# Performance work log

Hardware: AMD Instinct MI355X
Metric: run time of the kernel (lower is better)

The kernel has to match this reference:

```python
import jax, jax.numpy as jnp
import numpy as np

N_WIN = 8
NUM_HEADS = 8
TOPK = 4
D_MODEL = 128
SCALE = D_MODEL ** (-0.5)


def setup_inputs() -> dict:
    key = jax.random.key(0)
    k1, k2 = jax.random.split(key)
    cv_feature = jax.random.normal(k1, (1, 128, 128, 128), dtype=jnp.float32)
    mv_feature = jax.random.normal(k2, (1, 2, 128, 128, 128), dtype=jnp.float32)
    return {"cv_feature": cv_feature, "mv_feature": mv_feature}


def reference(cv_feature, mv_feature):
    # cv_feature: [N, H, W, C] query view; mv_feature: [N, V, H, W, C] multi-view KV
    N, H, W, C = cv_feature.shape
    V = mv_feature.shape[1]
    j = i = N_WIN
    h, w = H // j, W // i
    p2, w2 = j * i, h * w
    ch = C // NUM_HEADS  # per-head dim

    # window partition: n (j h) (i w) c -> n (j i) h w c
    cv_patch = cv_feature.reshape(N, j, h, i, w, C).transpose(0, 1, 3, 2, 4, 5).reshape(N, p2, h, w, C)
    mv_patch = mv_feature.reshape(N, V, j, h, i, w, C).transpose(0, 1, 2, 4, 3, 5, 6).reshape(N, V, p2, h, w, C)

    q_pix = cv_patch.reshape(N, p2, w2, C)          # [N, p2, w2, C]
    kv_pix = mv_patch.reshape(N, V, p2, w2, C)      # [N, V, p2, w2, C]

    # window-level descriptors (means) -> routing logits
    q_win = cv_patch.mean(axis=(2, 3))              # [N, p2, C]
    k_win = mv_patch.mean(axis=(3, 4))              # [N, V, p2, C]

    # TopK routing (detached in original; forward math identical)
    k_flat = k_win.reshape(N, V * p2, C)
    attn_logit = jnp.einsum('npc,nqc->npq', q_win * SCALE, k_flat)  # [N, p2, V*p2]
    topk_logit, r_idx = jax.lax.top_k(attn_logit, TOPK)
    r_weight = jax.nn.softmax(topk_logit, axis=-1)  # computed by module, unused downstream

    # KV gather of selected windows: [N, p2, topk, w2, C]
    kv_flat = kv_pix.reshape(N, V * p2, w2, C)
    kv_sel = kv_flat[jnp.arange(N)[:, None, None], r_idx]

    # per-window multi-head attention over topk*w2 gathered tokens
    q = q_pix.reshape(N, p2, w2, NUM_HEADS, ch)
    kv = kv_sel.reshape(N, p2, TOPK * w2, NUM_HEADS, ch)
    attn = jnp.einsum('npwmc,npxmc->npmwx', q * SCALE, kv)  # [N, p2, m, w2, topk*w2]
    attn = jax.nn.softmax(attn, axis=-1)
    out = jnp.einsum('npmwx,npxmc->npwmc', attn, kv)        # [N, p2, w2, m, ch]

    # merge windows back: n (j i) (h w) c -> n (j h) (i w) c
    out = out.reshape(N, j, i, h, w, C).transpose(0, 1, 3, 2, 4, 5).reshape(N, H, W, C)
    return out
```

## Files before the change

### kernel.cpp

```cpp
#include <hip/hip_runtime.h>

#define HH_ 128
#define WW_ 128
#define CC_ 128
#define P2 64
#define W2 256
#define NH 8
#define CH 16
#define NV 2
#define TOPK 4
#define SCALE 0.08838834764831845f
#define SCALE_L2E 0.1275216f
#define CLAMP_L2 28.8539f

typedef unsigned short u16;
typedef unsigned int   u32;
typedef short s8v __attribute__((ext_vector_type(8)));
typedef float f4  __attribute__((ext_vector_type(4)));

#if __has_builtin(__builtin_amdgcn_exp2f)
#define EXP2(x) __builtin_amdgcn_exp2f(x)
#else
#define EXP2(x) exp2f(x)
#endif

union FRAG { uint4 q; u32 u[4]; s8v v; };

__device__ float g_means[(P2 + NV * P2) * CC_];
__device__ int2  g_part[64];

__device__ inline u16 f2b(float v) {
    union { float f; u32 u; } x; x.f = v;
    u32 r = x.u + 0x7FFFu + ((x.u >> 16) & 1u);
    return (u16)(r >> 16);
}
__device__ inline float b2f(u16 h) {
    union { u32 u; float f; } x; x.u = (u32)h << 16; return x.f;
}
__device__ inline float h2f(u16 h) {
    u32 s = (h >> 15) & 1u, e = (h >> 10) & 31u, m = h & 1023u;
    float v;
    if (e == 0)       v = m * 5.9604644775e-8f;
    else if (e == 31) v = 65504.f;
    else { union { u32 u; float f; } x; x.u = ((e + 112u) << 23) | (m << 13); v = x.f; }
    return s ? -v : v;
}
__device__ inline u16 f2h(float v) {
    union { float f; u32 u; } x; x.f = v;
    u32 s = (x.u >> 16) & 0x8000u;
    int  e = (int)((x.u >> 23) & 0xFF) - 112;
    u32  m = x.u & 0x7FFFFF;
    if (e >= 31) return (u16)(s | 0x7BFF);
    if (e <= 0) {
        if (e < -10) return (u16)s;
        m |= 0x800000u;
        int sh = 14 - e;
        u32 r = m >> sh, rem = m & ((1u << sh) - 1u), half = 1u << (sh - 1);
        if (rem > half || (rem == half && (r & 1))) r++;
        return (u16)(s | r);
    }
    u32 r = ((u32)e << 10) | (m >> 13), rem = m & 0x1FFFu;
    if (rem > 0x1000u || (rem == 0x1000u && (r & 1))) r++;
    return (u16)(s | r);
}

__device__ inline u32 pkhi(float a, float b) {
    union { float f; u32 u; } xa, xb; xa.f = a; xb.f = b;
    return (xa.u >> 16) | (xb.u & 0xFFFF0000u);
}
__device__ inline float hipart(float a) {
    union { float f; u32 u; } x; x.f = a; x.u &= 0xFFFF0000u; return x.f;
}

__device__ inline int mode_from_parts() {
    int c0 = 0, c1 = 0;
#pragma unroll 8
    for (int k = 0; k < 64; ++k) { int2 v = g_part[k]; c0 += v.x; c1 += v.y; }
    const float T = 256.f * 64.f;
    float f0 = c0 / T, f1 = c1 / T;
    if (f1 >= 0.85f) return 1;
    if (f0 >= 0.80f) return 0;
    return 2;
}

template<int MODE>
__device__ inline float decode1(const void* __restrict__ src, int off) {
    if (MODE == 0) return ((const float*)src)[off];
    u16 h = ((const u16*)src)[off];
    return (MODE == 1) ? b2f(h) : h2f(h);
}

template<int MODE>
__device__ inline float4 loadf4(const void* __restrict__ src, int off) {
    if (MODE == 0) return *(const float4*)((const float*)src + off);
    uint2 v = *(const uint2*)((const u16*)src + off);
    float4 r;
    if (MODE == 1) {
        r.x = b2f((u16)v.x); r.y = b2f((u16)(v.x >> 16));
        r.z = b2f((u16)v.y); r.w = b2f((u16)(v.y >> 16));
    } else {
        r.x = h2f((u16)v.x); r.y = h2f((u16)(v.x >> 16));
        r.z = h2f((u16)v.y); r.w = h2f((u16)(v.y >> 16));
    }
    return r;
}

template<int MODE>
__device__ inline void store4t(void* __restrict__ out, int off, const float* __restrict__ r) {
    if (MODE == 0) {
        *(float4*)((float*)out + off) = make_float4(r[0], r[1], r[2], r[3]);
    } else if (MODE == 1) {
        u32 w0 = (u32)f2b(r[0]) | ((u32)f2b(r[1]) << 16);
        u32 w1 = (u32)f2b(r[2]) | ((u32)f2b(r[3]) << 16);
        *(uint2*)((u16*)out + off) = make_uint2(w0, w1);
    } else {
        u32 w0 = (u32)f2h(r[0]) | ((u32)f2h(r[1]) << 16);
        u32 w1 = (u32)f2h(r[2]) | ((u32)f2h(r[3]) << 16);
        *(uint2*)((u16*)out + off) = make_uint2(w0, w1);
    }
}

__global__ void detect_sample(const void* __restrict__ cv, int n) {
    __shared__ int bc[2];
    int tid = threadIdx.x, k = blockIdx.x;
    if (tid < 2) bc[tid] = 0;
    __syncthreads();
    int lim32 = n / 2;
    int lim16 = n / 2;
    u32 r = ((u32)(tid + k * 257) * 2654435761u);
    int j32 = (int)(r % (u32)lim32);
    float a = fabsf(((const float*)cv)[j32]);
    bool c0 = (a >= 1e-4f && a <= 1e4f);
    int j16 = 2 * (int)((r >> 8) % (u32)lim16);
    float b = fabsf(b2f(((const u16*)cv)[j16]));
    bool c1 = (b >= 1e-4f && b <= 1e4f);
    unsigned long long b0 = __ballot(c0);
    unsigned long long b1 = __ballot(c1);
    if ((tid & 63) == 0) {
        atomicAdd(&bc[0], __popcll(b0));
        atomicAdd(&bc[1], __popcll(b1));
    }
    __syncthreads();
    if (tid == 0) g_part[k] = make_int2(bc[0], bc[1]);
}

template<int MODE>
__device__ inline void wm_accum(const void* __restrict__ src, int voff, int jj, int ii,
                                int pc, int c0, float* __restrict__ acc) {
#pragma unroll
    for (int k = 0; k < 8; ++k) {
        int px = 8 * pc + k;
        int hh = px >> 4, ww = px & 15;
        int a = voff + ((jj * 16 + hh) * WW_ + ii * 16 + ww) * CC_ + c0;
        if (MODE == 0) {
            const float4* p4 = (const float4*)((const float*)src + a);
            float4 x = p4[0], y = p4[1];
            acc[0] += x.x; acc[1] += x.y; acc[2] += x.z; acc[3] += x.w;
            acc[4] += y.x; acc[5] += y.y; acc[6] += y.z; acc[7] += y.w;
        } else {
            uint4 v = *(const uint4*)((const u16*)src + a);
            u32 wd[4] = { v.x, v.y, v.z, v.w };
#pragma unroll
            for (int j = 0; j < 4; ++j) {
                u16 lo = (u16)(wd[j] & 0xFFFFu), hi = (u16)(wd[j] >> 16);
                acc[2 * j]     += (MODE == 1) ? b2f(lo) : h2f(lo);
                acc[2 * j + 1] += (MODE == 1) ? b2f(hi) : h2f(hi);
            }
        }
    }
}

__global__ __launch_bounds__(512) void win_mean_kernel(const void* __restrict__ cv,
                                                       const void* __restrict__ mv) {
    __shared__ float part[32][128];
    __shared__ int   smode;
    int row = blockIdx.x, tid = threadIdx.x;
    if (tid == 0) smode = mode_from_parts();
    __syncthreads();
    int mode = smode;
    int o = tid & 15, pc = tid >> 4;
    const void* src; int voff = 0; int p;
    if (row < P2) { p = row; src = cv; }
    else { int r = row - P2; voff = (r >> 6) * HH_ * WW_ * CC_; p = r & 63; src = mv; }
    int jj = p >> 3, ii = p & 7;
    int c0 = 8 * o;
    float acc[8];
#pragma unroll
    for (int j = 0; j < 8; ++j) acc[j] = 0.f;
    if (mode == 0)      wm_accum<0>(src, voff, jj, ii, pc, c0, acc);
    else if (mode == 1) wm_accum<1>(src, voff, jj, ii, pc, c0, acc);
    else                wm_accum<2>(src, voff, jj, ii, pc, c0, acc);
#pragma unroll
    for (int j = 0; j < 8; ++j) part[pc][c0 + j] = acc[j];
    __syncthreads();
    if (tid < 128) {
        float s = 0.f;
#pragma unroll
        for (int k = 0; k < 32; ++k) s += part[k][tid];
        g_means[row * CC_ + tid] = s * (1.0f / 256.0f);
    }
}

template<int MODE>
__device__ void attn_body(const void* __restrict__ cv, const void* __restrict__ mv,
                          void* __restrict__ out, int p, int m, int tid,
                          u32 (* __restrict__ kfrag)[64][4],
                          u32 (* __restrict__ vfrag)[64][4],
                          const int* __restrict__ rwin) {
    int jj = p >> 3, ii = p & 7;
    int wv = tid >> 6, l = tid & 63;
    int kh = wv >> 3, qs = wv & 7;
    int lg = l >> 4, lr = l & 15;

    FRAG qf1[2], qf2[2];
#pragma unroll
    for (int qi = 0; qi < 2; ++qi) {
        int qrow = qs * 32 + qi * 16 + lr;
        int hh = qrow >> 4, ww = qrow & 15;
        int pix = (jj * 16 + hh) * WW_ + (ii * 16 + ww);
        float4 qv = loadf4<MODE>(cv, pix * CC_ + m * CH + 4 * lg);
        float q0 = qv.x * SCALE_L2E, q1 = qv.y * SCALE_L2E;
        float q2 = qv.z * SCALE_L2E, q3 = qv.w * SCALE_L2E;
        u32 h01 = pkhi(q0, q1), h23 = pkhi(q2, q3);
        u32 l01 = pkhi(q0 - hipart(q0), q1 - hipart(q1));
        u32 l23 = pkhi(q2 - hipart(q2), q3 - hipart(q3));
        qf1[qi].u[0] = h01; qf1[qi].u[1] = h23; qf1[qi].u[2] = l01; qf1[qi].u[3] = l23;
        qf2[qi].u[0] = l01; qf2[qi].u[1] = l23; qf2[qi].u[2] = h01; qf2[qi].u[3] = h23;
    }

    auto stage = [&](int r) {
#pragma unroll
        for (int i = 0; i < 2; ++i) {
            int s = tid + i * 1024;
            int tl = s >> 6, sl = s & 63;
            int slg = sl >> 4, slr = sl & 15;
            int t = rwin[2 * r + (tl >> 4)];
            int v = t >> 6, pp = t & 63;
            int jj2 = pp >> 3, ii2 = pp & 7;
            int wrow = (v * HH_ + jj2 * 16 + (tl & 15)) * WW_ + ii2 * 16;
            {
                float4 kc = loadf4<MODE>(mv, (wrow + slr) * CC_ + m * CH + 4 * slg);
                FRAG kf;
                kf.u[0] = pkhi(kc.x, kc.y);
                kf.u[1] = pkhi(kc.z, kc.w);
                kf.u[2] = pkhi(kc.x - hipart(kc.x), kc.y - hipart(kc.y));
                kf.u[3] = pkhi(kc.z - hipart(kc.z), kc.w - hipart(kc.w));
                *(uint4*)&kfrag[tl][sl][0] = kf.q;
            }
            {
                int a = (wrow + 4 * slg) * CC_ + m * CH + slr;
                float v0 = decode1<MODE>(mv, a);
                float v1 = decode1<MODE>(mv, a + CC_);
                float v2 = decode1<MODE>(mv, a + 2 * CC_);
                float v3 = decode1<MODE>(mv, a + 3 * CC_);
                FRAG vf;
                vf.u[0] = pkhi(v0, v1);
                vf.u[1] = pkhi(v2, v3);
                vf.u[2] = pkhi(v0 - hipart(v0), v1 - hipart(v1));
                vf.u[3] = pkhi(v2 - hipart(v2), v3 - hipart(v3));
                *(uint4*)&vfrag[tl][sl][0] = vf.q;
            }
        }
    };

    f4 Oacc0 = {0.f, 0.f, 0.f, 0.f};
    f4 Oacc1 = {0.f, 0.f, 0.f, 0.f};
    float lp0 = 0.f, lp1 = 0.f;
    const uint4* kp = (const uint4*)&kfrag[kh * 16][0][0] + l;
    const uint4* vp = (const uint4*)&vfrag[kh * 16][0][0] + l;

    auto computeh = [&]() {
#pragma unroll 4
        for (int tl = 0; tl < 16; ++tl) {
            FRAG kf, vf;
            kf.q = kp[tl * 64];
            vf.q = vp[tl * 64];
            {
                f4 sc = {0.f, 0.f, 0.f, 0.f};
                sc = __builtin_amdgcn_mfma_f32_16x16x32_bf16(kf.v, qf1[0].v, sc, 0, 0, 0);
                sc = __builtin_amdgcn_mfma_f32_16x16x32_bf16(kf.v, qf2[0].v, sc, 0, 0, 0);
                float pe0 = EXP2(fminf(sc[0], CLAMP_L2));
                float pe1 = EXP2(fminf(sc[1], CLAMP_L2));
                float pe2 = EXP2(fminf(sc[2], CLAMP_L2));
                float pe3 = EXP2(fminf(sc[3], CLAMP_L2));
                lp0 += (hipart(pe0) + hipart(pe1)) + (hipart(pe2) + hipart(pe3));
                FRAG pf;
                pf.u[0] = pkhi(pe0, pe1);
                pf.u[1] = pkhi(pe2, pe3);
                pf.u[2] = pf.u[0];
                pf.u[3] = pf.u[1];
                Oacc0 = __builtin_amdgcn_mfma_f32_16x16x32_bf16(vf.v, pf.v, Oacc0, 0, 0, 0);
            }
            {
                f4 sc = {0.f, 0.f, 0.f, 0.f};
                sc = __builtin_amdgcn_mfma_f32_16x16x32_bf16(kf.v, qf1[1].v, sc, 0, 0, 0);
                sc = __builtin_amdgcn_mfma_f32_16x16x32_bf16(kf.v, qf2[1].v, sc, 0, 0, 0);
                float pe0 = EXP2(fminf(sc[0], CLAMP_L2));
                float pe1 = EXP2(fminf(sc[1], CLAMP_L2));
                float pe2 = EXP2(fminf(sc[2], CLAMP_L2));
                float pe3 = EXP2(fminf(sc[3], CLAMP_L2));
                lp1 += (hipart(pe0) + hipart(pe1)) + (hipart(pe2) + hipart(pe3));
                FRAG pf;
                pf.u[0] = pkhi(pe0, pe1);
                pf.u[1] = pkhi(pe2, pe3);
                pf.u[2] = pf.u[0];
                pf.u[3] = pf.u[1];
                Oacc1 = __builtin_amdgcn_mfma_f32_16x16x32_bf16(vf.v, pf.v, Oacc1, 0, 0, 0);
            }
        }
    };

    stage(0);
    __syncthreads();
    computeh();
    __syncthreads();
    stage(1);
    __syncthreads();
    computeh();
    __syncthreads();

    float* comb = (float*)&kfrag[0][0][0];
    int ci = (qs * 64 + l) * 10;
    if (kh == 1) {
#pragma unroll
        for (int r = 0; r < 4; ++r) { comb[ci + r] = Oacc0[r]; comb[ci + 4 + r] = Oacc1[r]; }
        comb[ci + 8] = lp0;
        comb[ci + 9] = lp1;
    }
    __syncthreads();
    if (kh == 0) {
#pragma unroll
        for (int r = 0; r < 4; ++r) { Oacc0[r] += comb[ci + r]; Oacc1[r] += comb[ci + 4 + r]; }
        lp0 += comb[ci + 8];
        lp1 += comb[ci + 9];
#pragma unroll
        for (int qi = 0; qi < 2; ++qi) {
            float lt = (qi == 0) ? lp0 : lp1;
            lt += __shfl_xor(lt, 16);
            lt += __shfl_xor(lt, 32);
            float inv = 1.0f / fmaxf(lt, 1e-30f);
            f4 Oa = (qi == 0) ? Oacc0 : Oacc1;
            float res[4];
#pragma unroll
            for (int r = 0; r < 4; ++r)
                res[r] = fminf(fmaxf(Oa[r] * inv, -1000.f), 1000.f);
            int qrow = qs * 32 + qi * 16 + lr;
            int hh = qrow >> 4, ww = qrow & 15;
            int pix = (jj * 16 + hh) * WW_ + (ii * 16 + ww);
            store4t<MODE>(out, pix * CC_ + m * CH + 4 * lg, res);
        }
    }
}

__global__ __launch_bounds__(1024, 8) void attn_kernel(const void* __restrict__ cv,
                                                       const void* __restrict__ mv,
                                                       void* __restrict__ out) {
    __shared__ u32 kfrag[32][64][4];
    __shared__ u32 vfrag[32][64][4];
    __shared__ float slog[NV * P2];
    __shared__ int   sridx[TOPK];
    __shared__ int   smode;

    int bid = blockIdx.x;
    int p = bid >> 3, m = bid & 7;
    int tid = threadIdx.x;

    {
        int t  = tid >> 3;
        int cs = (tid & 7) << 4;
        const float4* qw = (const float4*)(g_means + p * CC_ + cs);
        const float4* kw = (const float4*)(g_means + (P2 + t) * CC_ + cs);
        float a = 0.f;
#pragma unroll
        for (int i = 0; i < 4; ++i) {
            float4 qv = qw[i], kv4 = kw[i];
            a += qv.x * kv4.x + qv.y * kv4.y + qv.z * kv4.z + qv.w * kv4.w;
        }
        a += __shfl_down(a, 4, 8);
        a += __shfl_down(a, 2, 8);
        a += __shfl_down(a, 1, 8);
        if ((tid & 7) == 0) slog[t] = a;
    }
    __syncthreads();
    if (tid == 0) {
        smode = mode_from_parts();
#pragma unroll
        for (int k = 0; k < TOPK; ++k) {
            int best = 0; float bv = slog[0];
            for (int q2 = 1; q2 < NV * P2; ++q2)
                if (slog[q2] > bv) { bv = slog[q2]; best = q2; }
            sridx[k] = best;
            slog[best] = -3.0e38f;
        }
    }
    __syncthreads();

    int mode = smode;
    int rwin[TOPK];
#pragma unroll
    for (int k = 0; k < TOPK; ++k) rwin[k] = sridx[k] & 127;

    if (mode == 0)      attn_body<0>(cv, mv, out, p, m, tid, kfrag, vfrag, rwin);
    else if (mode == 1) attn_body<1>(cv, mv, out, p, m, tid, kfrag, vfrag, rwin);
    else                attn_body<2>(cv, mv, out, p, m, tid, kfrag, vfrag, rwin);
}

extern "C" void kernel_launch(void* const* d_in, const int* in_sizes, int n_in,
                              void* d_out, int out_size, void* d_ws, size_t ws_size,
                              hipStream_t stream) {
    const void* cv = d_in[0];
    const void* mv = d_in[1];
    int n_cv = in_sizes[0];
    if (n_in >= 2 && in_sizes[0] > in_sizes[1]) { cv = d_in[1]; mv = d_in[0]; n_cv = in_sizes[1]; }
    (void)d_ws; (void)ws_size; (void)out_size;

    detect_sample<<<64, 256, 0, stream>>>(cv, n_cv);
    win_mean_kernel<<<192, 512, 0, stream>>>(cv, mv);
    attn_kernel<<<P2 * NH, 1024, 0, stream>>>(cv, mv, d_out);
}
```

Measured before the change: 129.9 us.

## Fuse dtype detection, window means, and attention into one kernel with grid barriers

Merges the three launches (dtype sampling, window-mean reduction, routed attention) into a single persistent kernel. Global atomic counters in workspace act as grid-wide barriers between the phases, and a memset resets them on each call. This removes inter-kernel launch gaps at the cost of spin-waiting on atomics. It assumes all 512 blocks of 1024 threads are co-resident, otherwise the barriers can deadlock.

```diff
diff --git a/kernel.cpp b/kernel.cpp
--- a/kernel.cpp
+++ b/kernel.cpp
@@ -117,87 +117,6 @@
         u32 w0 = (u32)f2h(r[0]) | ((u32)f2h(r[1]) << 16);
         u32 w1 = (u32)f2h(r[2]) | ((u32)f2h(r[3]) << 16);
         *(uint2*)((u16*)out + off) = make_uint2(w0, w1);
-    }
-}
-
-__global__ void detect_sample(const void* __restrict__ cv, int n) {
-    __shared__ int bc[2];
-    int tid = threadIdx.x, k = blockIdx.x;
-    if (tid < 2) bc[tid] = 0;
-    __syncthreads();
-    int lim32 = n / 2;
-    int lim16 = n / 2;
-    u32 r = ((u32)(tid + k * 257) * 2654435761u);
-    int j32 = (int)(r % (u32)lim32);
-    float a = fabsf(((const float*)cv)[j32]);
-    bool c0 = (a >= 1e-4f && a <= 1e4f);
-    int j16 = 2 * (int)((r >> 8) % (u32)lim16);
-    float b = fabsf(b2f(((const u16*)cv)[j16]));
-    bool c1 = (b >= 1e-4f && b <= 1e4f);
-    unsigned long long b0 = __ballot(c0);
-    unsigned long long b1 = __ballot(c1);
-    if ((tid & 63) == 0) {
-        atomicAdd(&bc[0], __popcll(b0));
-        atomicAdd(&bc[1], __popcll(b1));
-    }
-    __syncthreads();
-    if (tid == 0) g_part[k] = make_int2(bc[0], bc[1]);
-}
-
-template<int MODE>
-__device__ inline void wm_accum(const void* __restrict__ src, int voff, int jj, int ii,
-                                int pc, int c0, float* __restrict__ acc) {
-#pragma unroll
-    for (int k = 0; k < 8; ++k) {
-        int px = 8 * pc + k;
-        int hh = px >> 4, ww = px & 15;
-        int a = voff + ((jj * 16 + hh) * WW_ + ii * 16 + ww) * CC_ + c0;
-        if (MODE == 0) {
-            const float4* p4 = (const float4*)((const float*)src + a);
-            float4 x = p4[0], y = p4[1];
-            acc[0] += x.x; acc[1] += x.y; acc[2] += x.z; acc[3] += x.w;
-            acc[4] += y.x; acc[5] += y.y; acc[6] += y.z; acc[7] += y.w;
-        } else {
-            uint4 v = *(const uint4*)((const u16*)src + a);
-            u32 wd[4] = { v.x, v.y, v.z, v.w };
-#pragma unroll
-            for (int j = 0; j < 4; ++j) {
-                u16 lo = (u16)(wd[j] & 0xFFFFu), hi = (u16)(wd[j] >> 16);
-                acc[2 * j]     += (MODE == 1) ? b2f(lo) : h2f(lo);
-                acc[2 * j + 1] += (MODE == 1) ? b2f(hi) : h2f(hi);
-            }
-        }
-    }
-}
-
-__global__ __launch_bounds__(512) void win_mean_kernel(const void* __restrict__ cv,
-                                                       const void* __restrict__ mv) {
-    __shared__ float part[32][128];
-    __shared__ int   smode;
-    int row = blockIdx.x, tid = threadIdx.x;
-    if (tid == 0) smode = mode_from_parts();
-    __syncthreads();
-    int mode = smode;
-    int o = tid & 15, pc = tid >> 4;
-    const void* src; int voff = 0; int p;
-    if (row < P2) { p = row; src = cv; }
-    else { int r = row - P2; voff = (r >> 6) * HH_ * WW_ * CC_; p = r & 63; src = mv; }
-    int jj = p >> 3, ii = p & 7;
-    int c0 = 8 * o;
-    float acc[8];
-#pragma unroll
-    for (int j = 0; j < 8; ++j) acc[j] = 0.f;
-    if (mode == 0)      wm_accum<0>(src, voff, jj, ii, pc, c0, acc);
-    else if (mode == 1) wm_accum<1>(src, voff, jj, ii, pc, c0, acc);
-    else                wm_accum<2>(src, voff, jj, ii, pc, c0, acc);
-#pragma unroll
-    for (int j = 0; j < 8; ++j) part[pc][c0 + j] = acc[j];
-    __syncthreads();
-    if (tid < 128) {
-        float s = 0.f;
-#pragma unroll
-        for (int k = 0; k < 32; ++k) s += part[k][tid];
-        g_means[row * CC_ + tid] = s * (1.0f / 256.0f);
     }
 }
 
@@ -352,6 +271,235 @@
     }
 }
 
+template<int MODE>
+__device__ inline void wm_row(const void* __restrict__ cv, const void* __restrict__ mv,
+                              int row, int tid, float (* __restrict__ wmpart)[128]) {
+    int o = tid & 15, pc = tid >> 4;
+    const void* src; int voff = 0; int p;
+    if (row < P2) { p = row; src = cv; }
+    else { int r = row - P2; voff = (r >> 6) * HH_ * WW_ * CC_; p = r & 63; src = mv; }
+    int jj = p >> 3, ii = p & 7;
+    int c0 = 8 * o;
+    float acc[8];
+#pragma unroll
+    for (int j = 0; j < 8; ++j) acc[j] = 0.f;
+#pragma unroll
+    for (int k = 0; k < 4; ++k) {
+        int px = 4 * pc + k;
+        int hh = px >> 4, ww = px & 15;
+        int a = voff + ((jj * 16 + hh) * WW_ + ii * 16 + ww) * CC_ + c0;
+        if (MODE == 0) {
+            const float4* p4 = (const float4*)((const float*)src + a);
+            float4 x = p4[0], y = p4[1];
+            acc[0] += x.x; acc[1] += x.y; acc[2] += x.z; acc[3] += x.w;
+            acc[4] += y.x; acc[5] += y.y; acc[6] += y.z; acc[7] += y.w;
+        } else {
+            uint4 v = *(const uint4*)((const u16*)src + a);
+            u32 wd[4] = { v.x, v.y, v.z, v.w };
+#pragma unroll
+            for (int j = 0; j < 4; ++j) {
+                u16 lo = (u16)(wd[j] & 0xFFFFu), hi = (u16)(wd[j] >> 16);
+                acc[2 * j]     += (MODE == 1) ? b2f(lo) : h2f(lo);
+                acc[2 * j + 1] += (MODE == 1) ? b2f(hi) : h2f(hi);
+            }
+        }
+    }
+#pragma unroll
+    for (int j = 0; j < 8; ++j) wmpart[pc][c0 + j] = acc[j];
+}
+
+__global__ __launch_bounds__(1024, 8) void fused_kernel(const void* __restrict__ cv,
+                                                        const void* __restrict__ mv,
+                                                        void* __restrict__ out,
+                                                        int* __restrict__ cnt, int n) {
+    __shared__ u32 kfrag[32][64][4];
+    __shared__ u32 vfrag[32][64][4];
+    __shared__ float slog[NV * P2];
+    __shared__ int   sridx[TOPK];
+    __shared__ int   smode;
+    __shared__ int   bc[2];
+
+    int bid = blockIdx.x, tid = threadIdx.x;
+    int p = bid >> 3, m = bid & 7;
+
+    if (bid < 64) {
+        if (tid < 2) bc[tid] = 0;
+        __syncthreads();
+        if (tid < 256) {
+            int lim = n / 2;
+            u32 r = ((u32)(tid + bid * 257) * 2654435761u);
+            int j32 = (int)(r % (u32)lim);
+            float a = fabsf(((const float*)cv)[j32]);
+            bool c0 = (a >= 1e-4f && a <= 1e4f);
+            int j16 = 2 * (int)((r >> 8) % (u32)lim);
+            float b = fabsf(b2f(((const u16*)cv)[j16]));
+            bool c1 = (b >= 1e-4f && b <= 1e4f);
+            unsigned long long b0 = __ballot(c0);
+            unsigned long long b1 = __ballot(c1);
+            if ((tid & 63) == 0) {
+                atomicAdd(&bc[0], __popcll(b0));
+                atomicAdd(&bc[1], __popcll(b1));
+            }
+        }
+        __syncthreads();
+        if (tid == 0) {
+            atomicAdd(&cnt[2], bc[0]);
+            atomicAdd(&cnt[3], bc[1]);
+            __threadfence();
+            atomicAdd(&cnt[0], 1);
+        }
+    }
+    if (tid == 0) {
+        while (atomicAdd(&cnt[0], 0) < 64) { __builtin_amdgcn_s_sleep(2); }
+        int c0s = atomicAdd(&cnt[2], 0);
+        int c1s = atomicAdd(&cnt[3], 0);
+        const float T = 256.f * 64.f;
+        float f0 = c0s / T, f1 = c1s / T;
+        smode = (f1 >= 0.85f) ? 1 : ((f0 >= 0.80f) ? 0 : 2);
+    }
+    __syncthreads();
+    int mode = smode;
+
+    if (bid < 192) {
+        float (*wmpart)[128] = (float(*)[128])&kfrag[0][0][0];
+        if (mode == 0)      wm_row<0>(cv, mv, bid, tid, wmpart);
+        else if (mode == 1) wm_row<1>(cv, mv, bid, tid, wmpart);
+        else                wm_row<2>(cv, mv, bid, tid, wmpart);
+        __syncthreads();
+        if (tid < 128) {
+            float s = 0.f;
+#pragma unroll
+            for (int k = 0; k < 64; ++k) s += wmpart[k][tid];
+            g_means[bid * CC_ + tid] = s * (1.0f / 256.0f);
+        }
+        __threadfence();
+        __syncthreads();
+        if (tid == 0) atomicAdd(&cnt[1], 1);
+    }
+    if (tid == 0) {
+        while (atomicAdd(&cnt[1], 0) < 192) { __builtin_amdgcn_s_sleep(2); }
+        __threadfence();
+    }
+    __syncthreads();
+
+    {
+        int t  = tid >> 3;
+        int cs = (tid & 7) << 4;
+        const float4* qw = (const float4*)(g_means + p * CC_ + cs);
+        const float4* kw = (const float4*)(g_means + (P2 + t) * CC_ + cs);
+        float a = 0.f;
+#pragma unroll
+        for (int i = 0; i < 4; ++i) {
+            float4 qv = qw[i], kv4 = kw[i];
+            a += qv.x * kv4.x + qv.y * kv4.y + qv.z * kv4.z + qv.w * kv4.w;
+        }
+        a += __shfl_down(a, 4, 8);
+        a += __shfl_down(a, 2, 8);
+        a += __shfl_down(a, 1, 8);
+        if ((tid & 7) == 0) slog[t] = a;
+    }
+    __syncthreads();
+    if (tid == 0) {
+#pragma unroll
+        for (int k = 0; k < TOPK; ++k) {
+            int best = 0; float bv = slog[0];
+            for (int q2 = 1; q2 < NV * P2; ++q2)
+                if (slog[q2] > bv) { bv = slog[q2]; best = q2; }
+            sridx[k] = best;
+            slog[best] = -3.0e38f;
+        }
+    }
+    __syncthreads();
+
+    int rwin[TOPK];
+#pragma unroll
+    for (int k = 0; k < TOPK; ++k) rwin[k] = sridx[k] & 127;
+
+    if (mode == 0)      attn_body<0>(cv, mv, out, p, m, tid, kfrag, vfrag, rwin);
+    else if (mode == 1) attn_body<1>(cv, mv, out, p, m, tid, kfrag, vfrag, rwin);
+    else                attn_body<2>(cv, mv, out, p, m, tid, kfrag, vfrag, rwin);
+}
+
+__global__ void detect_sample(const void* __restrict__ cv, int n) {
+    __shared__ int bc[2];
+    int tid = threadIdx.x, k = blockIdx.x;
+    if (tid < 2) bc[tid] = 0;
+    __syncthreads();
+    int lim = n / 2;
+    u32 r = ((u32)(tid + k * 257) * 2654435761u);
+    int j32 = (int)(r % (u32)lim);
+    float a = fabsf(((const float*)cv)[j32]);
+    bool c0 = (a >= 1e-4f && a <= 1e4f);
+    int j16 = 2 * (int)((r >> 8) % (u32)lim);
+    float b = fabsf(b2f(((const u16*)cv)[j16]));
+    bool c1 = (b >= 1e-4f && b <= 1e4f);
+    unsigned long long b0 = __ballot(c0);
+    unsigned long long b1 = __ballot(c1);
+    if ((tid & 63) == 0) {
+        atomicAdd(&bc[0], __popcll(b0));
+        atomicAdd(&bc[1], __popcll(b1));
+    }
+    __syncthreads();
+    if (tid == 0) g_part[k] = make_int2(bc[0], bc[1]);
+}
+
+template<int MODE>
+__device__ inline void wm_accum(const void* __restrict__ src, int voff, int jj, int ii,
+                                int pc, int c0, float* __restrict__ acc) {
+#pragma unroll
+    for (int k = 0; k < 8; ++k) {
+        int px = 8 * pc + k;
+        int hh = px >> 4, ww = px & 15;
+        int a = voff + ((jj * 16 + hh) * WW_ + ii * 16 + ww) * CC_ + c0;
+        if (MODE == 0) {
+            const float4* p4 = (const float4*)((const float*)src + a);
+            float4 x = p4[0], y = p4[1];
+            acc[0] += x.x; acc[1] += x.y; acc[2] += x.z; acc[3] += x.w;
+            acc[4] += y.x; acc[5] += y.y; acc[6] += y.z; acc[7] += y.w;
+        } else {
+            uint4 v = *(const uint4*)((const u16*)src + a);
+            u32 wd[4] = { v.x, v.y, v.z, v.w };
+#pragma unroll
+            for (int j = 0; j < 4; ++j) {
+                u16 lo = (u16)(wd[j] & 0xFFFFu), hi = (u16)(wd[j] >> 16);
+                acc[2 * j]     += (MODE == 1) ? b2f(lo) : h2f(lo);
+                acc[2 * j + 1] += (MODE == 1) ? b2f(hi) : h2f(hi);
+            }
+        }
+    }
+}
+
+__global__ __launch_bounds__(512) void win_mean_kernel2(const void* __restrict__ cv,
+                                                        const void* __restrict__ mv) {
+    __shared__ float part[32][128];
+    __shared__ int   smode;
+    int row = blockIdx.x, tid = threadIdx.x;
+    if (tid == 0) smode = mode_from_parts();
+    __syncthreads();
+    int mode = smode;
+    int o = tid & 15, pc = tid >> 4;
+    const void* src; int voff = 0; int p;
+    if (row < P2) { p = row; src = cv; }
+    else { int r = row - P2; voff = (r >> 6) * HH_ * WW_ * CC_; p = r & 63; src = mv; }
+    int jj = p >> 3, ii = p & 7;
+    int c0 = 8 * o;
+    float acc[8];
+#pragma unroll
+    for (int j = 0; j < 8; ++j) acc[j] = 0.f;
+    if (mode == 0)      wm_accum<0>(src, voff, jj, ii, pc, c0, acc);
+    else if (mode == 1) wm_accum<1>(src, voff, jj, ii, pc, c0, acc);
+    else                wm_accum<2>(src, voff, jj, ii, pc, c0, acc);
+#pragma unroll
+    for (int j = 0; j < 8; ++j) part[pc][c0 + j] = acc[j];
+    __syncthreads();
+    if (tid < 128) {
+        float s = 0.f;
+#pragma unroll
+        for (int k = 0; k < 32; ++k) s += part[k][tid];
+        g_means[row * CC_ + tid] = s * (1.0f / 256.0f);
+    }
+}
+
 __global__ __launch_bounds__(1024, 8) void attn_kernel(const void* __restrict__ cv,
                                                        const void* __restrict__ mv,
                                                        void* __restrict__ out) {
@@ -412,9 +560,15 @@
     const void* mv = d_in[1];
     int n_cv = in_sizes[0];
     if (n_in >= 2 && in_sizes[0] > in_sizes[1]) { cv = d_in[1]; mv = d_in[0]; n_cv = in_sizes[1]; }
-    (void)d_ws; (void)ws_size; (void)out_size;
-
-    detect_sample<<<64, 256, 0, stream>>>(cv, n_cv);
-    win_mean_kernel<<<192, 512, 0, stream>>>(cv, mv);
-    attn_kernel<<<P2 * NH, 1024, 0, stream>>>(cv, mv, d_out);
-}
+    (void)out_size;
+
+    if (d_ws != nullptr && ws_size >= 64) {
+        hipError_t e = hipMemsetAsync(d_ws, 0, 64, stream);
+        (void)e;
+        fused_kernel<<<P2 * NH, 1024, 0, stream>>>(cv, mv, d_out, (int*)d_ws, n_cv);
+    } else {
+        detect_sample<<<64, 256, 0, stream>>>(cv, n_cv);
+        win_mean_kernel2<<<192, 512, 0, stream>>>(cv, mv);
+        attn_kernel<<<P2 * NH, 1024, 0, stream>>>(cv, mv, d_out);
+    }
+}
```

New measurement: 208.2 us. +60.2%, slower.

## Warp-specialize attention: producer waves stage KV windows while consumer waves compute

Applied to the files above, without the earlier changes.

Replaces the two-phase stage/compute scheme, where all 16 waves staged two windows and then split keys across two halves before a shared-memory reduction, with warp specialization. Waves 8-15 stage the next selected window into a double-buffered LDS slot while waves 0-7 run the MFMA attention over the current one. Each compute wave now handles all four windows itself, so the cross-half combine step goes away. The trade-off is that only half the waves do MFMA work, so the serial compute chain per wave doubles, and there are four barrier-separated rounds instead of two phases.

```diff
diff --git a/kernel.cpp b/kernel.cpp
--- a/kernel.cpp
+++ b/kernel.cpp
@@ -125,13 +125,12 @@
     int tid = threadIdx.x, k = blockIdx.x;
     if (tid < 2) bc[tid] = 0;
     __syncthreads();
-    int lim32 = n / 2;
-    int lim16 = n / 2;
+    int lim = n / 2;
     u32 r = ((u32)(tid + k * 257) * 2654435761u);
-    int j32 = (int)(r % (u32)lim32);
+    int j32 = (int)(r % (u32)lim);
     float a = fabsf(((const float*)cv)[j32]);
     bool c0 = (a >= 1e-4f && a <= 1e4f);
-    int j16 = 2 * (int)((r >> 8) % (u32)lim16);
+    int j16 = 2 * (int)((r >> 8) % (u32)lim);
     float b = fabsf(b2f(((const u16*)cv)[j16]));
     bool c1 = (b >= 1e-4f && b <= 1e4f);
     unsigned long long b0 = __ballot(c0);
@@ -204,135 +203,124 @@
 template<int MODE>
 __device__ void attn_body(const void* __restrict__ cv, const void* __restrict__ mv,
                           void* __restrict__ out, int p, int m, int tid,
-                          u32 (* __restrict__ kfrag)[64][4],
-                          u32 (* __restrict__ vfrag)[64][4],
+                          u32 (* __restrict__ kfrag)[16][64][4],
+                          u32 (* __restrict__ vfrag)[16][64][4],
                           const int* __restrict__ rwin) {
     int jj = p >> 3, ii = p & 7;
     int wv = tid >> 6, l = tid & 63;
-    int kh = wv >> 3, qs = wv & 7;
+    int qs = wv & 7;
     int lg = l >> 4, lr = l & 15;
 
+    auto stage_slot = [&](int widx, int tl, int sl, int b) {
+        int slg = sl >> 4, slr = sl & 15;
+        int t = rwin[widx];
+        int v = t >> 6, pp = t & 63;
+        int jj2 = pp >> 3, ii2 = pp & 7;
+        int wrow = (v * HH_ + jj2 * 16 + tl) * WW_ + ii2 * 16;
+        {
+            float4 kc = loadf4<MODE>(mv, (wrow + slr) * CC_ + m * CH + 4 * slg);
+            FRAG kf;
+            kf.u[0] = pkhi(kc.x, kc.y);
+            kf.u[1] = pkhi(kc.z, kc.w);
+            kf.u[2] = pkhi(kc.x - hipart(kc.x), kc.y - hipart(kc.y));
+            kf.u[3] = pkhi(kc.z - hipart(kc.z), kc.w - hipart(kc.w));
+            *(uint4*)&kfrag[b][tl][sl][0] = kf.q;
+        }
+        {
+            int a = (wrow + 4 * slg) * CC_ + m * CH + slr;
+            float v0 = decode1<MODE>(mv, a);
+            float v1 = decode1<MODE>(mv, a + CC_);
+            float v2 = decode1<MODE>(mv, a + 2 * CC_);
+            float v3 = decode1<MODE>(mv, a + 3 * CC_);
+            FRAG vf;
+            vf.u[0] = pkhi(v0, v1);
+            vf.u[1] = pkhi(v2, v3);
+            vf.u[2] = pkhi(v0 - hipart(v0), v1 - hipart(v1));
+            vf.u[3] = pkhi(v2 - hipart(v2), v3 - hipart(v3));
+            *(uint4*)&vfrag[b][tl][sl][0] = vf.q;
+        }
+    };
+
     FRAG qf1[2], qf2[2];
-#pragma unroll
-    for (int qi = 0; qi < 2; ++qi) {
-        int qrow = qs * 32 + qi * 16 + lr;
-        int hh = qrow >> 4, ww = qrow & 15;
-        int pix = (jj * 16 + hh) * WW_ + (ii * 16 + ww);
-        float4 qv = loadf4<MODE>(cv, pix * CC_ + m * CH + 4 * lg);
-        float q0 = qv.x * SCALE_L2E, q1 = qv.y * SCALE_L2E;
-        float q2 = qv.z * SCALE_L2E, q3 = qv.w * SCALE_L2E;
-        u32 h01 = pkhi(q0, q1), h23 = pkhi(q2, q3);
-        u32 l01 = pkhi(q0 - hipart(q0), q1 - hipart(q1));
-        u32 l23 = pkhi(q2 - hipart(q2), q3 - hipart(q3));
-        qf1[qi].u[0] = h01; qf1[qi].u[1] = h23; qf1[qi].u[2] = l01; qf1[qi].u[3] = l23;
-        qf2[qi].u[0] = l01; qf2[qi].u[1] = l23; qf2[qi].u[2] = h01; qf2[qi].u[3] = h23;
-    }
-
-    auto stage = [&](int r) {
-#pragma unroll
-        for (int i = 0; i < 2; ++i) {
-            int s = tid + i * 1024;
-            int tl = s >> 6, sl = s & 63;
-            int slg = sl >> 4, slr = sl & 15;
-            int t = rwin[2 * r + (tl >> 4)];
-            int v = t >> 6, pp = t & 63;
-            int jj2 = pp >> 3, ii2 = pp & 7;
-            int wrow = (v * HH_ + jj2 * 16 + (tl & 15)) * WW_ + ii2 * 16;
-            {
-                float4 kc = loadf4<MODE>(mv, (wrow + slr) * CC_ + m * CH + 4 * slg);
-                FRAG kf;
-                kf.u[0] = pkhi(kc.x, kc.y);
-                kf.u[1] = pkhi(kc.z, kc.w);
-                kf.u[2] = pkhi(kc.x - hipart(kc.x), kc.y - hipart(kc.y));
-                kf.u[3] = pkhi(kc.z - hipart(kc.z), kc.w - hipart(kc.w));
-                *(uint4*)&kfrag[tl][sl][0] = kf.q;
-            }
-            {
-                int a = (wrow + 4 * slg) * CC_ + m * CH + slr;
-                float v0 = decode1<MODE>(mv, a);
-                float v1 = decode1<MODE>(mv, a + CC_);
-                float v2 = decode1<MODE>(mv, a + 2 * CC_);
-                float v3 = decode1<MODE>(mv, a + 3 * CC_);
-                FRAG vf;
-                vf.u[0] = pkhi(v0, v1);
-                vf.u[1] = pkhi(v2, v3);
-                vf.u[2] = pkhi(v0 - hipart(v0), v1 - hipart(v1));
-                vf.u[3] = pkhi(v2 - hipart(v2), v3 - hipart(v3));
-                *(uint4*)&vfrag[tl][sl][0] = vf.q;
-            }
-        }
-    };
+    if (wv < 8) {
+#pragma unroll
+        for (int qi = 0; qi < 2; ++qi) {
+            int qrow = qs * 32 + qi * 16 + lr;
+            int hh = qrow >> 4, ww = qrow & 15;
+            int pix = (jj * 16 + hh) * WW_ + (ii * 16 + ww);
+            float4 qv = loadf4<MODE>(cv, pix * CC_ + m * CH + 4 * lg);
+            float q0 = qv.x * SCALE_L2E, q1 = qv.y * SCALE_L2E;
+            float q2 = qv.z * SCALE_L2E, q3 = qv.w * SCALE_L2E;
+            u32 h01 = pkhi(q0, q1), h23 = pkhi(q2, q3);
+            u32 l01 = pkhi(q0 - hipart(q0), q1 - hipart(q1));
+            u32 l23 = pkhi(q2 - hipart(q2), q3 - hipart(q3));
+            qf1[qi].u[0] = h01; qf1[qi].u[1] = h23; qf1[qi].u[2] = l01; qf1[qi].u[3] = l23;
+            qf2[qi].u[0] = l01; qf2[qi].u[1] = l23; qf2[qi].u[2] = h01; qf2[qi].u[3] = h23;
+        }
+    }
+
+    stage_slot(0, tid >> 6, tid & 63, 0);
+    __syncthreads();
 
     f4 Oacc0 = {0.f, 0.f, 0.f, 0.f};
     f4 Oacc1 = {0.f, 0.f, 0.f, 0.f};
     float lp0 = 0.f, lp1 = 0.f;
-    const uint4* kp = (const uint4*)&kfrag[kh * 16][0][0] + l;
-    const uint4* vp = (const uint4*)&vfrag[kh * 16][0][0] + l;
-
-    auto computeh = [&]() {
+
+#pragma unroll 1
+    for (int r = 0; r < 4; ++r) {
+        if (wv >= 8) {
+            if (r < 3) {
+                int t2 = tid - 512;
+                stage_slot(r + 1, t2 >> 6, t2 & 63, (r + 1) & 1);
+                int t3 = t2 + 512;
+                stage_slot(r + 1, t3 >> 6, t3 & 63, (r + 1) & 1);
+            }
+        } else {
+            const uint4* kp = (const uint4*)&kfrag[r & 1][0][0][0] + l;
+            const uint4* vp = (const uint4*)&vfrag[r & 1][0][0][0] + l;
 #pragma unroll 4
-        for (int tl = 0; tl < 16; ++tl) {
-            FRAG kf, vf;
-            kf.q = kp[tl * 64];
-            vf.q = vp[tl * 64];
-            {
-                f4 sc = {0.f, 0.f, 0.f, 0.f};
-                sc = __builtin_amdgcn_mfma_f32_16x16x32_bf16(kf.v, qf1[0].v, sc, 0, 0, 0);
-                sc = __builtin_amdgcn_mfma_f32_16x16x32_bf16(kf.v, qf2[0].v, sc, 0, 0, 0);
-                float pe0 = EXP2(fminf(sc[0], CLAMP_L2));
-                float pe1 = EXP2(fminf(sc[1], CLAMP_L2));
-                float pe2 = EXP2(fminf(sc[2], CLAMP_L2));
-                float pe3 = EXP2(fminf(sc[3], CLAMP_L2));
-                lp0 += (hipart(pe0) + hipart(pe1)) + (hipart(pe2) + hipart(pe3));
-                FRAG pf;
-                pf.u[0] = pkhi(pe0, pe1);
-                pf.u[1] = pkhi(pe2, pe3);
-                pf.u[2] = pf.u[0];
-                pf.u[3] = pf.u[1];
-                Oacc0 = __builtin_amdgcn_mfma_f32_16x16x32_bf16(vf.v, pf.v, Oacc0, 0, 0, 0);
+            for (int tl = 0; tl < 16; ++tl) {
+                FRAG kf, vf;
+                kf.q = kp[tl * 64];
+                vf.q = vp[tl * 64];
+                {
+                    f4 sc = {0.f, 0.f, 0.f, 0.f};
+                    sc = __builtin_amdgcn_mfma_f32_16x16x32_bf16(kf.v, qf1[0].v, sc, 0, 0, 0);
+                    sc = __builtin_amdgcn_mfma_f32_16x16x32_bf16(kf.v, qf2[0].v, sc, 0, 0, 0);
+                    float pe0 = EXP2(fminf(sc[0], CLAMP_L2));
+                    float pe1 = EXP2(fminf(sc[1], CLAMP_L2));
+                    float pe2 = EXP2(fminf(sc[2], CLAMP_L2));
+                    float pe3 = EXP2(fminf(sc[3], CLAMP_L2));
+                    lp0 += (hipart(pe0) + hipart(pe1)) + (hipart(pe2) + hipart(pe3));
+                    FRAG pf;
+                    pf.u[0] = pkhi(pe0, pe1);
+                    pf.u[1] = pkhi(pe2, pe3);
+                    pf.u[2] = pf.u[0];
+                    pf.u[3] = pf.u[1];
+                    Oacc0 = __builtin_amdgcn_mfma_f32_16x16x32_bf16(vf.v, pf.v, Oacc0, 0, 0, 0);
+                }
+                {
+                    f4 sc = {0.f, 0.f, 0.f, 0.f};
+                    sc = __builtin_amdgcn_mfma_f32_16x16x32_bf16(kf.v, qf1[1].v, sc, 0, 0, 0);
+                    sc = __builtin_amdgcn_mfma_f32_16x16x32_bf16(kf.v, qf2[1].v, sc, 0, 0, 0);
+                    float pe0 = EXP2(fminf(sc[0], CLAMP_L2));
+                    float pe1 = EXP2(fminf(sc[1], CLAMP_L2));
+                    float pe2 = EXP2(fminf(sc[2], CLAMP_L2));
+                    float pe3 = EXP2(fminf(sc[3], CLAMP_L2));
+                    lp1 += (hipart(pe0) + hipart(pe1)) + (hipart(pe2) + hipart(pe3));
+                    FRAG pf;
+                    pf.u[0] = pkhi(pe0, pe1);
+                    pf.u[1] = pkhi(pe2, pe3);
+                    pf.u[2] = pf.u[0];
+                    pf.u[3] = pf.u[1];
+                    Oacc1 = __builtin_amdgcn_mfma_f32_16x16x32_bf16(vf.v, pf.v, Oacc1, 0, 0, 0);
+                }
             }
-            {
-                f4 sc = {0.f, 0.f, 0.f, 0.f};
-                sc = __builtin_amdgcn_mfma_f32_16x16x32_bf16(kf.v, qf1[1].v, sc, 0, 0, 0);
-                sc = __builtin_amdgcn_mfma_f32_16x16x32_bf16(kf.v, qf2[1].v, sc, 0, 0, 0);
-                float pe0 = EXP2(fminf(sc[0], CLAMP_L2));
-                float pe1 = EXP2(fminf(sc[1], CLAMP_L2));
-                float pe2 = EXP2(fminf(sc[2], CLAMP_L2));
-                float pe3 = EXP2(fminf(sc[3], CLAMP_L2));
-                lp1 += (hipart(pe0) + hipart(pe1)) + (hipart(pe2) + hipart(pe3));
-                FRAG pf;
-                pf.u[0] = pkhi(pe0, pe1);
-                pf.u[1] = pkhi(pe2, pe3);
-                pf.u[2] = pf.u[0];
-                pf.u[3] = pf.u[1];
-                Oacc1 = __builtin_amdgcn_mfma_f32_16x16x32_bf16(vf.v, pf.v, Oacc1, 0, 0, 0);
-            }
-        }
-    };
-
-    stage(0);
-    __syncthreads();
-    computeh();
-    __syncthreads();
-    stage(1);
-    __syncthreads();
-    computeh();
-    __syncthreads();
-
-    float* comb = (float*)&kfrag[0][0][0];
-    int ci = (qs * 64 + l) * 10;
-    if (kh == 1) {
-#pragma unroll
-        for (int r = 0; r < 4; ++r) { comb[ci + r] = Oacc0[r]; comb[ci + 4 + r] = Oacc1[r]; }
-        comb[ci + 8] = lp0;
-        comb[ci + 9] = lp1;
-    }
-    __syncthreads();
-    if (kh == 0) {
-#pragma unroll
-        for (int r = 0; r < 4; ++r) { Oacc0[r] += comb[ci + r]; Oacc1[r] += comb[ci + 4 + r]; }
-        lp0 += comb[ci + 8];
-        lp1 += comb[ci + 9];
+        }
+        __syncthreads();
+    }
+
+    if (wv < 8) {
 #pragma unroll
         for (int qi = 0; qi < 2; ++qi) {
             float lt = (qi == 0) ? lp0 : lp1;
@@ -355,8 +343,8 @@
 __global__ __launch_bounds__(1024, 8) void attn_kernel(const void* __restrict__ cv,
                                                        const void* __restrict__ mv,
                                                        void* __restrict__ out) {
-    __shared__ u32 kfrag[32][64][4];
-    __shared__ u32 vfrag[32][64][4];
+    __shared__ u32 kfrag[2][16][64][4];
+    __shared__ u32 vfrag[2][16][64][4];
     __shared__ float slog[NV * P2];
     __shared__ int   sridx[TOPK];
     __shared__ int   smode;
```

New measurement: 127.0 us. 2.3% less time.
